# Kernel tuning notes

Measured on AMD Instinct MI355X. Metric: run time of the kernel, lower is better.

Reference implementation:

```python
import jax, jax.numpy as jnp
import numpy as np

ALPHA = 100.0   # norse SuperSpike surrogate-gradient sharpness (default)
DT = 0.001      # norse LIFBoxParameters default dt

@jax.custom_vjp
def heaviside(x):
    # spike function with SuperSpike surrogate gradient (norse method='super')
    return (x > 0).astype(x.dtype)

def _hs_fwd(x):
    return (x > 0).astype(x.dtype), x

def _hs_bwd(x, g):
    return (g / (ALPHA * jnp.abs(x) + 1.0) ** 2,)

heaviside.defvjp(_hs_fwd, _hs_bwd)


def setup_inputs() -> dict:
    key = jax.random.key(0)
    k0, k1, k2, k3, k4 = jax.random.split(key, 5)
    B, F, T = 256, 10, 8192
    inputs = jax.random.normal(k0, (B, F, T), dtype=jnp.float32)
    # learned scalar LIF parameters (one per parallel temporal layer)
    tau = jnp.array([200.0, 300.0, 600.0], dtype=jnp.float32)   # tau_mem_inv
    v_th = jnp.array([0.006, 0.008, 0.013], dtype=jnp.float32)  # thresholds
    conv_w = jax.random.normal(k1, (1, 3, 1, 1), dtype=jnp.float32) * 0.5
    conv_b = jax.random.normal(k2, (1,), dtype=jnp.float32) * 0.1
    lin_w = jax.random.normal(k3, (2, 10), dtype=jnp.float32) * 0.3
    lin_b = jax.random.normal(k4, (2,), dtype=jnp.float32) * 0.1
    return {"inputs": inputs, "tau": tau, "v_th": v_th,
            "conv_w": conv_w, "conv_b": conv_b, "lin_w": lin_w, "lin_b": lin_b}


def reference(inputs, tau, v_th, conv_w, conv_b, lin_w, lin_b):
    # inputs: [B, F, T]
    B, F, T = inputs.shape
    x_t = jnp.transpose(inputs, (2, 0, 1))          # [T, B, F], time-major
    tau3 = tau[:, None, None]                        # [3,1,1] broadcast over B,F
    vth3 = v_th[:, None, None]
    v0 = jnp.zeros((3, B, F), dtype=inputs.dtype)    # v_leak = 0 initial state

    def step(v, x):
        # LIFBox dynamics: dv = dt * tau_inv * (v_leak - v + i), v_leak=v_reset=0
        v = v + DT * tau3 * (x[None, :, :] - v)      # [3,B,F]
        z = heaviside(v - vth3)                      # spikes
        v = (1.0 - z) * v                            # reset to v_reset=0 on spike
        return v, z

    _, zs = jax.lax.scan(step, v0, x_t)              # zs: [T, 3, B, F]
    resp = jnp.transpose(zs, (2, 1, 3, 0))           # [B, 3, F, T]

    # 1x1 Conv2d over the 3 LIF channels -> [B, F, T]
    conv = jnp.einsum('bcft,c->bft', resp, conv_w[0, :, 0, 0]) + conv_b[0]
    # Linear over feature dim F=10 -> 2, output [B, 2, T]
    out = jnp.einsum('bft,of->bot', conv, lin_w) + lin_b[None, :, None]
    return out
```

## Files before the change

kernel.cpp:

```cpp
#include <hip/hip_runtime.h>


#define T_LEN 8192
#define NF 10
#define NSEQ 30
#define CHUNK 512
#define WARM 256
#define NCHUNKS 16
#define WWIN (WARM / 32)
#define MWIN (CHUNK / 32)

__device__ __forceinline__ float lif_step(float xx, float v, float k, float vt, bool& s) {
  float d  = __fsub_rn(xx, v);
  float p  = __fmul_rn(k, d);
  float vn = __fadd_rn(v, p);
  s = vn > vt;
  return s ? 0.0f : vn;
}

__device__ __forceinline__ void sim_warm(const float4 buf[8], float& v, float k, float vt) {
#pragma unroll
  for (int i = 0; i < 8; ++i) {
    bool s;
    v = lif_step(buf[i].x, v, k, vt, s);
    v = lif_step(buf[i].y, v, k, vt, s);
    v = lif_step(buf[i].z, v, k, vt, s);
    v = lif_step(buf[i].w, v, k, vt, s);
  }
}

__device__ __forceinline__ void sim_main(const float4 buf[8], float& v, float k, float vt,
                                         int tt, unsigned& mA, unsigned& mB) {
#pragma unroll
  for (int i = 0; i < 8; ++i) {
    float xs[4] = {buf[i].x, buf[i].y, buf[i].z, buf[i].w};
#pragma unroll
    for (int r = 0; r < 4; ++r) {
      bool s;
      v = lif_step(xs[r], v, k, vt, s);
      unsigned long long ub = __ballot(s);
      const int t = i * 4 + r;
      if (tt == t) {
        mA = (unsigned)(ub & 0xffffffffull);
        mB = (unsigned)(ub >> 32);
      }
    }
  }
}

__device__ __forceinline__ float lut_sum(unsigned m, const float* lut, int o, float bias) {
  float acc = bias;
#pragma unroll
  for (int g = 0; g < 6; ++g) {
    unsigned val = (m >> (5 * g)) & 31u;
    acc += lut[(g * 2 + o) * 32 + val];
  }
  return acc;
}

__global__ __launch_bounds__(64, 2) void lif_chunked(
    const float* __restrict__ x,
    const float* __restrict__ tau,
    const float* __restrict__ vth,
    const float* __restrict__ convw,
    const float* __restrict__ convb,
    const float* __restrict__ linw,
    const float* __restrict__ linb,
    float* __restrict__ out)
{
  const int b    = blockIdx.x;
  const int cb   = blockIdx.y;
  const int lane = threadIdx.x;
  const int half = lane >> 5;
  const int j    = lane & 31;
  const bool active = j < NSEQ;
  const int c = active ? j / NF : 0;
  const int f = active ? j % NF : 0;

  __shared__ float lut[384];
#pragma unroll
  for (int e = 0; e < 6; ++e) {
    int id = lane + 64 * e;
    int g = id >> 6, rem = id & 63, oo = rem >> 5, val = rem & 31;
    float sacc = 0.0f;
#pragma unroll
    for (int p = 0; p < 5; ++p) {
      if (val & (1 << p)) {
        int jj = 5 * g + p;
        sacc += convw[jj / NF] * linw[oo * NF + (jj % NF)];
      }
    }
    lut[id] = sacc;
  }
  __syncthreads();

  const float k  = __fmul_rn(0.001f, tau[c]);
  const float vt = active ? vth[c] : 3.0e38f;
  const int chunk = cb * 2 + half;
  const int t0 = chunk * CHUNK;
  const int ts = (chunk == 0) ? 0 : (t0 - WARM);

  const float* xrow = x + ((size_t)b * NF + f) * (size_t)T_LEN;
  const float4* pw = (const float4*)(xrow + ts);
  const float4* pm = (const float4*)(xrow + t0);

  const int o  = half;
  const int tt = j;
  float wsum = 0.0f;
#pragma unroll
  for (int f2 = 0; f2 < NF; ++f2) wsum += linw[o * NF + f2];
  const float bias = linb[o] + convb[0] * wsum;

  const int tA = 2 * cb * CHUNK;
  float* outA = out + ((size_t)b * 2 + o) * T_LEN + tA;
  float* outB = outA + CHUNK;

  float v = 0.0f;
  float4 bufA[8], bufB[8];
#pragma unroll
  for (int i = 0; i < 8; ++i) bufA[i] = pw[i];

#pragma unroll 1
  for (int w = 0; w < WWIN; w += 2) {
#pragma unroll
    for (int i = 0; i < 8; ++i) bufB[i] = pw[(w + 1) * 8 + i];
    sim_warm(bufA, v, k, vt);
    {
      const float4* nxt = (w + 2 < WWIN) ? (pw + (w + 2) * 8) : pm;
#pragma unroll
      for (int i = 0; i < 8; ++i) bufA[i] = nxt[i];
    }
    sim_warm(bufB, v, k, vt);
  }
  v = (chunk == 0) ? 0.0f : v;

#pragma unroll 1
  for (int w = 0; w < MWIN; w += 2) {
    unsigned mA = 0, mB = 0;
#pragma unroll
    for (int i = 0; i < 8; ++i) bufB[i] = pm[(w + 1) * 8 + i];
    sim_main(bufA, v, k, vt, tt, mA, mB);
    outA[w * 32 + tt] = lut_sum(mA, lut, o, bias);
    outB[w * 32 + tt] = lut_sum(mB, lut, o, bias);

    unsigned mA2 = 0, mB2 = 0;
    if (w + 2 < MWIN) {
#pragma unroll
      for (int i = 0; i < 8; ++i) bufA[i] = pm[(w + 2) * 8 + i];
    }
    sim_main(bufB, v, k, vt, tt, mA2, mB2);
    outA[(w + 1) * 32 + tt] = lut_sum(mA2, lut, o, bias);
    outB[(w + 1) * 32 + tt] = lut_sum(mB2, lut, o, bias);
  }
}

extern "C" void kernel_launch(void* const* d_in, const int* in_sizes, int n_in,
                              void* d_out, int out_size, void* d_ws, size_t ws_size,
                              hipStream_t stream) {
  const float* x     = (const float*)d_in[0];
  const float* tau   = (const float*)d_in[1];
  const float* vthp  = (const float*)d_in[2];
  const float* convw = (const float*)d_in[3];
  const float* convb = (const float*)d_in[4];
  const float* linw  = (const float*)d_in[5];
  const float* linb  = (const float*)d_in[6];
  float* out = (float*)d_out;

  const int B = in_sizes[0] / (NF * T_LEN);
  lif_chunked<<<dim3(B, NCHUNKS / 2), dim3(64), 0, stream>>>(
      x, tau, vthp, convw, convb, linw, linb, out);
}
```

Measured before the change: 157.8 us.

## Stage input windows through swizzled shared memory with cooperative coalesced loads

Each thread used to read its own time-series row straight from global memory as eight float4 per window, so accesses were strided across lanes. Now the whole wavefront loads the 20 rows cooperatively: consecutive lanes fetch consecutive float4s, three per lane. The data goes into a double-buffered shared-memory tile with an XOR swizzle to avoid bank conflicts, and each thread reads its row back from shared memory. Register buffers shrink from 16 float4 to a small rolling window, which may raise occupancy, but the single loop now pays per-window LDS writes plus a branch between warm-up and main phases.

Measured after the change: 150.2 us. -4.8%, faster.

```diff
diff --git a/kernel.cpp b/kernel.cpp
--- a/kernel.cpp
+++ b/kernel.cpp
@@ -7,8 +7,10 @@
 #define CHUNK 512
 #define WARM 256
 #define NCHUNKS 16
-#define WWIN (WARM / 32)
-#define MWIN (CHUNK / 32)
+#define NWIN 24
+#define WWIN 8
+#define NROW 20
+#define BUF4 (NROW * 8)
 
 __device__ __forceinline__ float lif_step(float xx, float v, float k, float vt, bool& s) {
   float d  = __fsub_rn(xx, v);
@@ -16,36 +18,6 @@
   float vn = __fadd_rn(v, p);
   s = vn > vt;
   return s ? 0.0f : vn;
-}
-
-__device__ __forceinline__ void sim_warm(const float4 buf[8], float& v, float k, float vt) {
-#pragma unroll
-  for (int i = 0; i < 8; ++i) {
-    bool s;
-    v = lif_step(buf[i].x, v, k, vt, s);
-    v = lif_step(buf[i].y, v, k, vt, s);
-    v = lif_step(buf[i].z, v, k, vt, s);
-    v = lif_step(buf[i].w, v, k, vt, s);
-  }
-}
-
-__device__ __forceinline__ void sim_main(const float4 buf[8], float& v, float k, float vt,
-                                         int tt, unsigned& mA, unsigned& mB) {
-#pragma unroll
-  for (int i = 0; i < 8; ++i) {
-    float xs[4] = {buf[i].x, buf[i].y, buf[i].z, buf[i].w};
-#pragma unroll
-    for (int r = 0; r < 4; ++r) {
-      bool s;
-      v = lif_step(xs[r], v, k, vt, s);
-      unsigned long long ub = __ballot(s);
-      const int t = i * 4 + r;
-      if (tt == t) {
-        mA = (unsigned)(ub & 0xffffffffull);
-        mB = (unsigned)(ub >> 32);
-      }
-    }
-  }
 }
 
 __device__ __forceinline__ float lut_sum(unsigned m, const float* lut, int o, float bias) {
@@ -78,6 +50,7 @@
   const int f = active ? j % NF : 0;
 
   __shared__ float lut[384];
+  __shared__ float4 xbuf[2][BUF4];
 #pragma unroll
   for (int e = 0; e < 6; ++e) {
     int id = lane + 64 * e;
@@ -97,12 +70,27 @@
   const float k  = __fmul_rn(0.001f, tau[c]);
   const float vt = active ? vth[c] : 3.0e38f;
   const int chunk = cb * 2 + half;
-  const int t0 = chunk * CHUNK;
-  const int ts = (chunk == 0) ? 0 : (t0 - WARM);
 
-  const float* xrow = x + ((size_t)b * NF + f) * (size_t)T_LEN;
-  const float4* pw = (const float4*)(xrow + ts);
-  const float4* pm = (const float4*)(xrow + t0);
+  const int srow = half * NF + f;
+  const int sw   = srow & 7;
+  const float4* rbase = &xbuf[0][srow * 8];
+
+  const float4* gp[3];
+  float4*       lp[3];
+  int           adj[3];
+#pragma unroll
+  for (int i = 0; i < 3; ++i) {
+    int id  = (i == 0) ? lane : (i == 1) ? (lane + 64) : ((lane & 31) + 128);
+    int row = id >> 3;
+    int q   = id & 7;
+    int h   = row / NF;
+    int fr  = row % NF;
+    int ch  = 2 * cb + h;
+    int ts  = (ch == 0) ? 0 : ch * CHUNK - WARM;
+    gp[i]  = (const float4*)(x + ((size_t)b * NF + fr) * (size_t)T_LEN + ts) + q;
+    lp[i]  = &xbuf[0][row * 8 + (q ^ (row & 7))];
+    adj[i] = (ch == 0) ? -(WARM / 4) : 0;
+  }
 
   const int o  = half;
   const int tt = j;
@@ -115,42 +103,76 @@
   float* outA = out + ((size_t)b * 2 + o) * T_LEN + tA;
   float* outB = outA + CHUNK;
 
+  {
+    float4 s0 = gp[0][0], s1 = gp[1][0], s2 = gp[2][0];
+    *lp[0] = s0; *lp[1] = s1; *lp[2] = s2;
+    gp[0] += 8; gp[1] += 8; gp[2] += 8;
+  }
+
   float v = 0.0f;
-  float4 bufA[8], bufB[8];
-#pragma unroll
-  for (int i = 0; i < 8; ++i) bufA[i] = pw[i];
 
 #pragma unroll 1
-  for (int w = 0; w < WWIN; w += 2) {
+  for (int w = 0; w < NWIN; ++w) {
+    const bool haveNext = (w + 1 < NWIN);
+    float4 s0, s1, s2;
+    if (haveNext) {
+      if (w + 1 == WWIN) {
+        gp[0] += adj[0]; gp[1] += adj[1]; gp[2] += adj[2];
+      }
+      s0 = gp[0][0]; s1 = gp[1][0]; s2 = gp[2][0];
+      gp[0] += 8; gp[1] += 8; gp[2] += 8;
+    }
+
+    const float4* rp = rbase + (w & 1) * BUF4;
+
+    if (w < WWIN) {
+      float4 x0 = rp[0 ^ sw];
+      float4 x1 = rp[1 ^ sw];
 #pragma unroll
-    for (int i = 0; i < 8; ++i) bufB[i] = pw[(w + 1) * 8 + i];
-    sim_warm(bufA, v, k, vt);
-    {
-      const float4* nxt = (w + 2 < WWIN) ? (pw + (w + 2) * 8) : pm;
+      for (int q = 0; q < 8; ++q) {
+        float4 xn = x1;
+        if (q + 2 < 8) xn = rp[(q + 2) ^ sw];
+        bool s;
+        v = lif_step(x0.x, v, k, vt, s);
+        v = lif_step(x0.y, v, k, vt, s);
+        v = lif_step(x0.z, v, k, vt, s);
+        v = lif_step(x0.w, v, k, vt, s);
+        x0 = x1; x1 = xn;
+      }
+      if (w == WWIN - 1) v = (chunk == 0) ? 0.0f : v;
+    } else {
+      unsigned mA = 0, mB = 0;
+      float4 x0 = rp[0 ^ sw];
+      float4 x1 = rp[1 ^ sw];
 #pragma unroll
-      for (int i = 0; i < 8; ++i) bufA[i] = nxt[i];
+      for (int q = 0; q < 8; ++q) {
+        float4 xn = x1;
+        if (q + 2 < 8) xn = rp[(q + 2) ^ sw];
+        float xs[4] = {x0.x, x0.y, x0.z, x0.w};
+#pragma unroll
+        for (int r = 0; r < 4; ++r) {
+          bool s;
+          v = lif_step(xs[r], v, k, vt, s);
+          unsigned long long ub = __ballot(s);
+          const int t = q * 4 + r;
+          if (tt == t) {
+            mA = (unsigned)(ub & 0xffffffffull);
+            mB = (unsigned)(ub >> 32);
+          }
+        }
+        x0 = x1; x1 = xn;
+      }
+      const int ow = w - WWIN;
+      outA[ow * 32 + tt] = lut_sum(mA, lut, o, bias);
+      outB[ow * 32 + tt] = lut_sum(mB, lut, o, bias);
     }
-    sim_warm(bufB, v, k, vt);
-  }
-  v = (chunk == 0) ? 0.0f : v;
 
-#pragma unroll 1
-  for (int w = 0; w < MWIN; w += 2) {
-    unsigned mA = 0, mB = 0;
-#pragma unroll
-    for (int i = 0; i < 8; ++i) bufB[i] = pm[(w + 1) * 8 + i];
-    sim_main(bufA, v, k, vt, tt, mA, mB);
-    outA[w * 32 + tt] = lut_sum(mA, lut, o, bias);
-    outB[w * 32 + tt] = lut_sum(mB, lut, o, bias);
-
-    unsigned mA2 = 0, mB2 = 0;
-    if (w + 2 < MWIN) {
-#pragma unroll
-      for (int i = 0; i < 8; ++i) bufA[i] = pm[(w + 2) * 8 + i];
+    if (haveNext) {
+      const int nb = (w + 1) & 1;
+      *(lp[0] + nb * BUF4) = s0;
+      *(lp[1] + nb * BUF4) = s1;
+      *(lp[2] + nb * BUF4) = s2;
     }
-    sim_main(bufB, v, k, vt, tt, mA2, mB2);
-    outA[(w + 1) * 32 + tt] = lut_sum(mA2, lut, o, bias);
-    outB[(w + 1) * 32 + tt] = lut_sum(mB2, lut, o, bias);
   }
 }
 
```
